# Optimization experiments

Hardware: AMD Instinct MI355X
Metric: run time of the kernel (lower is better)

Reference implementation:

```python
import jax, jax.numpy as jnp
import numpy as np
import math

EMBED_DIM = 256
N_HEAD = 8
N_LEVELS = 4
N_POINTS = 4
HEAD_DIM = EMBED_DIM // N_HEAD
TOTAL_POINTS = N_HEAD * N_LEVELS * N_POINTS
SPATIAL = np.array([[100, 100], [50, 50], [25, 25], [13, 13]], dtype=np.int32)
BS = 2
LEN_Q = int(SPATIAL.prod(1).sum())  # 13294, encoder self-attention
LEN_V = LEN_Q


def setup_inputs() -> dict:
    key = jax.random.key(0)
    ks = jax.random.split(key, 12)
    s = 1.0 / math.sqrt(EMBED_DIM)
    inp = {
        'query': jax.random.normal(ks[0], (BS, LEN_Q, EMBED_DIM), jnp.float32),
        'reference_points': jax.random.uniform(ks[1], (BS, LEN_Q, N_LEVELS, 2), jnp.float32),
        'value': jax.random.normal(ks[2], (BS, LEN_V, EMBED_DIM), jnp.float32),
        'value_spatial_shapes': jnp.asarray(SPATIAL),
        'W_value': jax.random.normal(ks[3], (EMBED_DIM, EMBED_DIM), jnp.float32) * s,
        'b_value': jnp.zeros((EMBED_DIM,), jnp.float32),
        'W_off': jax.random.normal(ks[4], (TOTAL_POINTS * 2, EMBED_DIM), jnp.float32) * 0.01,
        'b_off': jax.random.normal(ks[5], (TOTAL_POINTS * 2,), jnp.float32),
        'W_attn': jax.random.normal(ks[6], (TOTAL_POINTS, EMBED_DIM), jnp.float32) * s,
        'b_attn': jnp.zeros((TOTAL_POINTS,), jnp.float32),
        'W_out': jax.random.normal(ks[7], (EMBED_DIM, EMBED_DIM), jnp.float32) * s,
        'b_out': jnp.zeros((EMBED_DIM,), jnp.float32),
        'zeta': jnp.ones((1, 1, 1, HEAD_DIM), jnp.float32),  # search_type='embed'
    }
    return inp


def _grid_sample_bilinear(img, gx, gy):
    """img: [B,H,W,c]; gx,gy: [B,Q,P] normalized to [-1,1].
    align_corners=False, padding_mode='zeros' (matches F.grid_sample)."""
    B, H, W, c = img.shape
    x = (gx + 1.0) * (0.5 * W) - 0.5
    y = (gy + 1.0) * (0.5 * H) - 0.5
    x0 = jnp.floor(x)
    y0 = jnp.floor(y)
    wx = (x - x0)[..., None]
    wy = (y - y0)[..., None]
    flat = img.reshape(B, H * W, c)

    def gather(xi, yi):
        m = (xi >= 0) & (xi < W) & (yi >= 0) & (yi < H)
        xi_c = jnp.clip(xi, 0, W - 1).astype(jnp.int32)
        yi_c = jnp.clip(yi, 0, H - 1).astype(jnp.int32)
        idx = (yi_c * W + xi_c).reshape(B, -1, 1)
        v = jnp.take_along_axis(flat, idx, axis=1).reshape(B, *xi.shape[1:], c)
        return v * m[..., None]

    v00 = gather(x0, y0)
    v01 = gather(x0 + 1, y0)
    v10 = gather(x0, y0 + 1)
    v11 = gather(x0 + 1, y0 + 1)
    return (v00 * (1 - wx) * (1 - wy) + v01 * wx * (1 - wy)
            + v10 * (1 - wx) * wy + v11 * wx * wy)


def reference(query, reference_points, value, value_spatial_shapes,
              W_value, b_value, W_off, b_off, W_attn, b_attn, W_out, b_out, zeta):
    bs, Len_q, _ = query.shape
    Len_v = value.shape[1]
    shapes = np.asarray(value_spatial_shapes)  # static ints

    # value projection + sparse gate (zeta, not pruned/searched)
    v = value @ W_value.T + b_value
    v = v.reshape(bs, Len_v, N_HEAD, HEAD_DIM) * zeta  # [bs,Lv,h,c]

    # sampling offsets and attention weights from query
    off = (query @ W_off.T + b_off).reshape(bs, Len_q, N_HEAD, N_LEVELS, N_POINTS, 2)
    attn = (query @ W_attn.T + b_attn).reshape(bs, Len_q, N_HEAD, N_LEVELS * N_POINTS)
    attn = jax.nn.softmax(attn, axis=-1).reshape(bs, Len_q, N_HEAD, N_LEVELS, N_POINTS)

    # reference_points last dim == 2 branch
    normalizer = jnp.asarray(shapes[:, ::-1], jnp.float32).reshape(1, 1, 1, N_LEVELS, 1, 2)  # (W,H)
    loc = reference_points.reshape(bs, Len_q, 1, N_LEVELS, 1, 2) + off / normalizer
    grids = 2.0 * loc - 1.0  # [bs,Lq,h,L,P,2]

    B = bs * N_HEAD
    out = jnp.zeros((B, Len_q, HEAD_DIM), jnp.float32)
    start = 0
    for lvl in range(N_LEVELS):
        h, w = int(shapes[lvl, 0]), int(shapes[lvl, 1])
        # [bs, h*w, nh, c] -> [bs*nh, h, w, c]
        v_l = v[:, start:start + h * w].transpose(0, 2, 1, 3).reshape(B, h, w, HEAD_DIM)
        g = grids[:, :, :, lvl].transpose(0, 2, 1, 3, 4).reshape(B, Len_q, N_POINTS, 2)
        samp = _grid_sample_bilinear(v_l, g[..., 0], g[..., 1])  # [B,Lq,P,c]
        a_l = attn[:, :, :, lvl].transpose(0, 2, 1, 3).reshape(B, Len_q, N_POINTS)
        out = out + jnp.einsum('bqpc,bqp->bqc', samp, a_l)
        start += h * w

    out = out.reshape(bs, N_HEAD, Len_q, HEAD_DIM).transpose(0, 2, 1, 3).reshape(bs, Len_q, EMBED_DIM)
    return out @ W_out.T + b_out
```

## Files before the change

### kernel.cpp

```cpp
#include <hip/hip_runtime.h>


#define LQ    13294
#define NTOK  26588
#define CHUNK 3324
#define NE    6806528

typedef unsigned short ushort_t;
typedef __attribute__((ext_vector_type(8))) short short8;
typedef __attribute__((ext_vector_type(4))) float float4_t;
typedef __attribute__((ext_vector_type(2))) unsigned int uint2_t;

__device__ __forceinline__ ushort_t f2b(float f) {
    unsigned int x = __float_as_uint(f);
    return (ushort_t)((x + 0x7fffu + ((x >> 16) & 1u)) >> 16);
}

__device__ __forceinline__ void cvt_seg(const float* __restrict__ s,
                                        ushort_t* __restrict__ d,
                                        int n4, int gid, int stride) {
    const float4_t* s4 = (const float4_t*)s;
    for (int i = gid; i < n4; i += stride) {
        float4_t f = s4[i];
        ushort4 o;
        o.x = f2b(f.x); o.y = f2b(f.y); o.z = f2b(f.z); o.w = f2b(f.w);
        *(ushort4*)(d + (long)i * 4) = o;
    }
}

__global__ __launch_bounds__(256) void cvt_k(
    const float* q, const float* v, const float* Wv, const float* Wo,
    const float* Wa, const float* Wout,
    ushort_t* q_bf, ushort_t* v_bf, ushort_t* Wv_bf, ushort_t* WoWa_bf,
    ushort_t* Wout_bf)
{
    const int gid = blockIdx.x * 256 + threadIdx.x;
    const int stride = gridDim.x * 256;
    cvt_seg(q,    q_bf,            NE / 4,     gid, stride);
    cvt_seg(v,    v_bf,            NE / 4,     gid, stride);
    cvt_seg(Wv,   WoWa_bf ? Wv_bf : Wv_bf, 65536 / 4, gid, stride);
    cvt_seg(Wo,   WoWa_bf,         65536 / 4,  gid, stride);
    cvt_seg(Wa,   WoWa_bf + 65536, 32768 / 4,  gid, stride);
    cvt_seg(Wout, Wout_bf,         65536 / 4,  gid, stride);
}

__device__ __forceinline__ void gemm_tile(
    const ushort_t* __restrict__ A,
    const ushort_t* __restrict__ W,
    int m0, int n0, int M,
    ushort_t* As, ushort_t* Bs, float4_t acc[2][4])
{
    const int tid = threadIdx.x;
    const int w  = tid >> 6;
    const int ln = tid & 63;
    const int sr = tid >> 2;
    const int sc = (tid & 3) * 8;

    for (int k0 = 0; k0 < 256; k0 += 32) {
        #pragma unroll
        for (int rr = 0; rr < 128; rr += 64) {
            int m = m0 + sr + rr;
            short8 pk = {};
            if (m < M) pk = *(const short8*)(A + (long)m * 256 + k0 + sc);
            *(short8*)(As + (sr + rr) * 40 + sc) = pk;
        }
        *(short8*)(Bs + sr * 40 + sc) =
            *(const short8*)(W + (long)(n0 + sr) * 256 + k0 + sc);
        __syncthreads();

        const int krow = (ln >> 4) * 8;
        short8 af[2], bfr[4];
        #pragma unroll
        for (int i = 0; i < 2; i++)
            af[i] = *(const short8*)(As + (w * 32 + i * 16 + (ln & 15)) * 40 + krow);
        #pragma unroll
        for (int j = 0; j < 4; j++)
            bfr[j] = *(const short8*)(Bs + (j * 16 + (ln & 15)) * 40 + krow);
        #pragma unroll
        for (int i = 0; i < 2; i++)
            #pragma unroll
            for (int j = 0; j < 4; j++)
                acc[i][j] = __builtin_amdgcn_mfma_f32_16x16x32_bf16(af[i], bfr[j], acc[i][j], 0, 0, 0);
        __syncthreads();
    }
}

__global__ __launch_bounds__(256) void gemm_fused_k(
    const ushort_t* __restrict__ q_bf, const ushort_t* __restrict__ v_bf,
    const ushort_t* __restrict__ Wv,   const ushort_t* __restrict__ WoWa,
    const float* __restrict__ b_value, const float* __restrict__ b_off,
    const float* __restrict__ b_attn,  const float* __restrict__ zeta,
    ushort_t* __restrict__ vproj, float* __restrict__ oa)
{
    __shared__ __align__(16) ushort_t As[128 * 40];
    __shared__ __align__(16) ushort_t Bs[64 * 40];

    const int z = blockIdx.z;
    const int bid = blockIdx.x;
    int x, y;
    if (z == 0) {
        if (bid >= 832) return;
        int id = (bid & 7) * 104 + (bid >> 3);
        x = id >> 2; y = id & 3;
    } else {
        int id = (bid & 7) * 156 + (bid >> 3);
        x = id / 6; y = id - x * 6;
    }
    const int m0 = x * 128;
    const int n0 = y * 64;
    const ushort_t* A = z ? q_bf : v_bf;
    const ushort_t* W = z ? WoWa : Wv;

    float4_t acc[2][4] = {};
    gemm_tile(A, W, m0, n0, NTOK, As, Bs, acc);

    const int tid = threadIdx.x;
    const int w = tid >> 6, ln = tid & 63;
    const int col = ln & 15;
    const int rq  = (ln >> 4) * 4;
    #pragma unroll
    for (int j = 0; j < 4; j++) {
        int n = n0 + j * 16 + col;
        if (z == 0) {
            float bz = b_value[n];
            float zz = zeta[n & 31];
            #pragma unroll
            for (int i = 0; i < 2; i++) {
                #pragma unroll
                for (int r = 0; r < 4; r++) {
                    int m = m0 + w * 32 + i * 16 + rq + r;
                    if (m < NTOK) vproj[(long)m * 256 + n] = f2b((acc[i][j][r] + bz) * zz);
                }
            }
        } else {
            float bz = (n < 256) ? b_off[n] : b_attn[n - 256];
            #pragma unroll
            for (int i = 0; i < 2; i++) {
                #pragma unroll
                for (int r = 0; r < 4; r++) {
                    int m = m0 + w * 32 + i * 16 + rq + r;
                    if (m < NTOK) oa[(long)m * 384 + n] = acc[i][j][r] + bz;
                }
            }
        }
    }
}

__global__ __launch_bounds__(256) void gemm_out_k(
    const ushort_t* __restrict__ A,
    const ushort_t* __restrict__ W,
    const float* __restrict__ bias,
    float* __restrict__ C)
{
    __shared__ __align__(16) ushort_t As[128 * 40];
    __shared__ __align__(16) ushort_t Bs[64 * 40];

    const int bid = blockIdx.x;
    int id = (bid & 7) * 104 + (bid >> 3);
    const int m0 = (id >> 2) * 128;
    const int n0 = (id & 3) * 64;

    float4_t acc[2][4] = {};
    gemm_tile(A, W, m0, n0, NTOK, As, Bs, acc);

    const int tid = threadIdx.x;
    const int w = tid >> 6, ln = tid & 63;
    const int col = ln & 15;
    const int rq  = (ln >> 4) * 4;
    #pragma unroll
    for (int j = 0; j < 4; j++) {
        int n = n0 + j * 16 + col;
        float bz = bias[n];
        #pragma unroll
        for (int i = 0; i < 2; i++) {
            #pragma unroll
            for (int r = 0; r < 4; r++) {
                int m = m0 + w * 32 + i * 16 + rq + r;
                if (m < NTOK) C[(long)m * 256 + n] = acc[i][j][r] + bz;
            }
        }
    }
}

__global__ __launch_bounds__(512) void sample_k(
    const float* __restrict__ refp,
    const ushort_t* __restrict__ v,
    const float* __restrict__ oa,
    ushort_t* __restrict__ outp)
{
    __shared__ int   p_ofs[128][4];
    __shared__ float p_w[128][4];
    const int bid = blockIdx.x;
    const int t = (bid & 7) * CHUNK + (bid >> 3);
    if (t >= NTOK) return;
    const int b = (t >= LQ) ? 1 : 0;
    const int tid = threadIdx.x;

    if (tid < 128) {
        const int h = tid >> 4, pi = tid & 15;
        const int lvl = pi >> 2;
        const int Wi  = (lvl == 0) ? 100 : (lvl == 1) ? 50 : (lvl == 2) ? 25 : 13;
        const int st  = (lvl == 0) ? 0 : (lvl == 1) ? 10000 : (lvl == 2) ? 12500 : 13125;
        const float Wf = (float)Wi;

        float lg = oa[(long)t * 384 + 256 + h * 16 + pi];
        float smax = lg;
        #pragma unroll
        for (int d = 1; d < 16; d <<= 1) smax = fmaxf(smax, __shfl_xor(smax, d, 64));
        float ex = __expf(lg - smax);
        float sm = ex;
        #pragma unroll
        for (int d = 1; d < 16; d <<= 1) sm += __shfl_xor(sm, d, 64);
        const float a = ex / sm;

        float ox = oa[(long)t * 384 + h * 32 + pi * 2];
        float oy = oa[(long)t * 384 + h * 32 + pi * 2 + 1];
        float rx = refp[(long)t * 8 + lvl * 2];
        float ry = refp[(long)t * 8 + lvl * 2 + 1];

        float x = rx * Wf + ox - 0.5f;
        float y = ry * Wf + oy - 0.5f;
        float xf = floorf(x), yf = floorf(y);
        float wx = x - xf, wy = y - yf;
        int x0 = (int)xf, y0 = (int)yf;

        float mx0 = ((unsigned)x0       < (unsigned)Wi) ? (1.f - wx) : 0.f;
        float mx1 = ((unsigned)(x0 + 1) < (unsigned)Wi) ? wx         : 0.f;
        float my0 = ((unsigned)y0       < (unsigned)Wi) ? (1.f - wy) * a : 0.f;
        float my1 = ((unsigned)(y0 + 1) < (unsigned)Wi) ? wy * a         : 0.f;
        int x0c = min(max(x0, 0), Wi - 1);
        int x1c = min(max(x0 + 1, 0), Wi - 1);
        int y0c = min(max(y0, 0), Wi - 1);
        int y1c = min(max(y0 + 1, 0), Wi - 1);

        int r0 = st + y0c * Wi, r1 = st + y1c * Wi;
        p_ofs[tid][0] = (r0 + x0c) << 9;
        p_ofs[tid][1] = (r0 + x1c) << 9;
        p_ofs[tid][2] = (r1 + x0c) << 9;
        p_ofs[tid][3] = (r1 + x1c) << 9;
        p_w[tid][0] = mx0 * my0;
        p_w[tid][1] = mx1 * my0;
        p_w[tid][2] = mx0 * my1;
        p_w[tid][3] = mx1 * my1;
    }
    __syncthreads();

    const int h = tid >> 6, ln = tid & 63, g = ln & 7, s = ln >> 3;
    const char* vb = (const char*)(v + ((long)b * LQ) * 256 + h * 32 + g * 4);
    float4_t acc = {0.f, 0.f, 0.f, 0.f};

    #pragma unroll
    for (int it = 0; it < 2; it++) {
        const int task = h * 16 + it * 8 + s;
        int4     o  = *(const int4*)p_ofs[task];
        float4_t w4 = *(const float4_t*)p_w[task];
        uint2_t u00 = *(const uint2_t*)(vb + o.x);
        uint2_t u01 = *(const uint2_t*)(vb + o.y);
        uint2_t u10 = *(const uint2_t*)(vb + o.z);
        uint2_t u11 = *(const uint2_t*)(vb + o.w);
        acc[0] += w4.x * __uint_as_float(u00.x << 16)
                + w4.y * __uint_as_float(u01.x << 16)
                + w4.z * __uint_as_float(u10.x << 16)
                + w4.w * __uint_as_float(u11.x << 16);
        acc[1] += w4.x * __uint_as_float(u00.x & 0xffff0000u)
                + w4.y * __uint_as_float(u01.x & 0xffff0000u)
                + w4.z * __uint_as_float(u10.x & 0xffff0000u)
                + w4.w * __uint_as_float(u11.x & 0xffff0000u);
        acc[2] += w4.x * __uint_as_float(u00.y << 16)
                + w4.y * __uint_as_float(u01.y << 16)
                + w4.z * __uint_as_float(u10.y << 16)
                + w4.w * __uint_as_float(u11.y << 16);
        acc[3] += w4.x * __uint_as_float(u00.y & 0xffff0000u)
                + w4.y * __uint_as_float(u01.y & 0xffff0000u)
                + w4.z * __uint_as_float(u10.y & 0xffff0000u)
                + w4.w * __uint_as_float(u11.y & 0xffff0000u);
    }

    #pragma unroll
    for (int d = 32; d >= 8; d >>= 1) {
        acc.x += __shfl_down(acc.x, d, 64);
        acc.y += __shfl_down(acc.y, d, 64);
        acc.z += __shfl_down(acc.z, d, 64);
        acc.w += __shfl_down(acc.w, d, 64);
    }
    if (s == 0) {
        ushort4 o;
        o.x = f2b(acc.x); o.y = f2b(acc.y); o.z = f2b(acc.z); o.w = f2b(acc.w);
        *(ushort4*)(outp + (long)t * 256 + h * 32 + g * 4) = o;
    }
}

extern "C" void kernel_launch(void* const* d_in, const int* in_sizes, int n_in,
                              void* d_out, int out_size, void* d_ws, size_t ws_size,
                              hipStream_t stream)
{
    char* ws = (char*)d_ws;
    ushort_t* vproj   = (ushort_t*)ws;
    float*    oa      = (float*)(ws + (long)NE * 2);
    ushort_t* q_bf    = (ushort_t*)(ws + (long)NE * 2 + (long)NTOK * 1536);
    ushort_t* outpre  = q_bf;
    ushort_t* v_bf    = q_bf + NE;
    ushort_t* Wv_bf   = v_bf + NE;
    ushort_t* WoWa_bf = Wv_bf + 65536;
    ushort_t* Wout_bf = WoWa_bf + 98304;

    cvt_k<<<1024, 256, 0, stream>>>(
        (const float*)d_in[0], (const float*)d_in[2], (const float*)d_in[4],
        (const float*)d_in[6], (const float*)d_in[8], (const float*)d_in[10],
        q_bf, v_bf, Wv_bf, WoWa_bf, Wout_bf);

    gemm_fused_k<<<dim3(1248, 1, 2), 256, 0, stream>>>(
        q_bf, v_bf, Wv_bf, WoWa_bf,
        (const float*)d_in[5], (const float*)d_in[7], (const float*)d_in[9],
        (const float*)d_in[12], vproj, oa);

    sample_k<<<8 * CHUNK, 512, 0, stream>>>(
        (const float*)d_in[1], vproj, oa, outpre);

    gemm_out_k<<<832, 256, 0, stream>>>(
        outpre, Wout_bf, (const float*)d_in[11], (float*)d_out);
}
```

Before: 242.0 us.

## Load GEMM tiles directly to LDS and batch four tokens per sampling block

The GEMM tile loader now uses global_load_lds to move 16-byte chunks straight from global memory into unpadded LDS tiles. This removes the register round-trip and the M bounds check, so the last tile reads rows past NTOK from adjacent workspace memory, though its stores stay guarded. The unpadded row stride of 32 may also cause LDS bank conflicts on fragment reads. The sampling kernel now handles four tokens per 512-thread block, so every thread computes sampling offsets and weights and each lane accumulates eight points instead of two, with a shorter shuffle reduction.

```diff
diff --git a/kernel.cpp b/kernel.cpp
--- a/kernel.cpp
+++ b/kernel.cpp
@@ -3,7 +3,6 @@
 
 #define LQ    13294
 #define NTOK  26588
-#define CHUNK 3324
 #define NE    6806528
 
 typedef unsigned short ushort_t;
@@ -14,6 +13,12 @@
 __device__ __forceinline__ ushort_t f2b(float f) {
     unsigned int x = __float_as_uint(f);
     return (ushort_t)((x + 0x7fffu + ((x >> 16) & 1u)) >> 16);
+}
+
+__device__ __forceinline__ void gload16(const void* g, void* l) {
+    __builtin_amdgcn_global_load_lds(
+        (const __attribute__((address_space(1))) unsigned int*)g,
+        (__attribute__((address_space(3))) unsigned int*)l, 16, 0, 0);
 }
 
 __device__ __forceinline__ void cvt_seg(const float* __restrict__ s,
@@ -38,7 +43,7 @@
     const int stride = gridDim.x * 256;
     cvt_seg(q,    q_bf,            NE / 4,     gid, stride);
     cvt_seg(v,    v_bf,            NE / 4,     gid, stride);
-    cvt_seg(Wv,   WoWa_bf ? Wv_bf : Wv_bf, 65536 / 4, gid, stride);
+    cvt_seg(Wv,   Wv_bf,           65536 / 4,  gid, stride);
     cvt_seg(Wo,   WoWa_bf,         65536 / 4,  gid, stride);
     cvt_seg(Wa,   WoWa_bf + 65536, 32768 / 4,  gid, stride);
     cvt_seg(Wout, Wout_bf,         65536 / 4,  gid, stride);
@@ -47,35 +52,38 @@
 __device__ __forceinline__ void gemm_tile(
     const ushort_t* __restrict__ A,
     const ushort_t* __restrict__ W,
-    int m0, int n0, int M,
+    int m0, int n0,
     ushort_t* As, ushort_t* Bs, float4_t acc[2][4])
 {
     const int tid = threadIdx.x;
     const int w  = tid >> 6;
     const int ln = tid & 63;
-    const int sr = tid >> 2;
-    const int sc = (tid & 3) * 8;
+    const int lr = ln >> 2;
+    const int lc = (ln & 3) * 8;
+
+    ushort_t* lA0 = As + (w * 2 + 0) * 512;
+    ushort_t* lA1 = As + (w * 2 + 1) * 512;
+    ushort_t* lB  = Bs + w * 512;
+    const ushort_t* gA0 = A + (long)(m0 + w * 32 + lr) * 256 + lc;
+    const ushort_t* gA1 = gA0 + 16 * 256;
+    const ushort_t* gB  = W + (long)(n0 + w * 16 + lr) * 256 + lc;
+
+    const int krow = (ln >> 4) * 8;
+    const int fr   = ln & 15;
 
     for (int k0 = 0; k0 < 256; k0 += 32) {
-        #pragma unroll
-        for (int rr = 0; rr < 128; rr += 64) {
-            int m = m0 + sr + rr;
-            short8 pk = {};
-            if (m < M) pk = *(const short8*)(A + (long)m * 256 + k0 + sc);
-            *(short8*)(As + (sr + rr) * 40 + sc) = pk;
-        }
-        *(short8*)(Bs + sr * 40 + sc) =
-            *(const short8*)(W + (long)(n0 + sr) * 256 + k0 + sc);
+        gload16(gA0 + k0, lA0);
+        gload16(gA1 + k0, lA1);
+        gload16(gB  + k0, lB);
         __syncthreads();
 
-        const int krow = (ln >> 4) * 8;
         short8 af[2], bfr[4];
         #pragma unroll
         for (int i = 0; i < 2; i++)
-            af[i] = *(const short8*)(As + (w * 32 + i * 16 + (ln & 15)) * 40 + krow);
+            af[i] = *(const short8*)(As + (w * 32 + i * 16 + fr) * 32 + krow);
         #pragma unroll
         for (int j = 0; j < 4; j++)
-            bfr[j] = *(const short8*)(Bs + (j * 16 + (ln & 15)) * 40 + krow);
+            bfr[j] = *(const short8*)(Bs + (j * 16 + fr) * 32 + krow);
         #pragma unroll
         for (int i = 0; i < 2; i++)
             #pragma unroll
@@ -92,8 +100,8 @@
     const float* __restrict__ b_attn,  const float* __restrict__ zeta,
     ushort_t* __restrict__ vproj, float* __restrict__ oa)
 {
-    __shared__ __align__(16) ushort_t As[128 * 40];
-    __shared__ __align__(16) ushort_t Bs[64 * 40];
+    __shared__ __align__(16) ushort_t As[128 * 32];
+    __shared__ __align__(16) ushort_t Bs[64 * 32];
 
     const int z = blockIdx.z;
     const int bid = blockIdx.x;
@@ -108,11 +116,9 @@
     }
     const int m0 = x * 128;
     const int n0 = y * 64;
-    const ushort_t* A = z ? q_bf : v_bf;
-    const ushort_t* W = z ? WoWa : Wv;
 
     float4_t acc[2][4] = {};
-    gemm_tile(A, W, m0, n0, NTOK, As, Bs, acc);
+    gemm_tile(z ? q_bf : v_bf, z ? WoWa : Wv, m0, n0, As, Bs, acc);
 
     const int tid = threadIdx.x;
     const int w = tid >> 6, ln = tid & 63;
@@ -152,8 +158,8 @@
     const float* __restrict__ bias,
     float* __restrict__ C)
 {
-    __shared__ __align__(16) ushort_t As[128 * 40];
-    __shared__ __align__(16) ushort_t Bs[64 * 40];
+    __shared__ __align__(16) ushort_t As[128 * 32];
+    __shared__ __align__(16) ushort_t Bs[64 * 32];
 
     const int bid = blockIdx.x;
     int id = (bid & 7) * 104 + (bid >> 3);
@@ -161,7 +167,7 @@
     const int n0 = (id & 3) * 64;
 
     float4_t acc[2][4] = {};
-    gemm_tile(A, W, m0, n0, NTOK, As, Bs, acc);
+    gemm_tile(A, W, m0, n0, As, Bs, acc);
 
     const int tid = threadIdx.x;
     const int w = tid >> 6, ln = tid & 63;
@@ -188,22 +194,21 @@
     const float* __restrict__ oa,
     ushort_t* __restrict__ outp)
 {
-    __shared__ int   p_ofs[128][4];
-    __shared__ float p_w[128][4];
-    const int bid = blockIdx.x;
-    const int t = (bid & 7) * CHUNK + (bid >> 3);
-    if (t >= NTOK) return;
-    const int b = (t >= LQ) ? 1 : 0;
+    __shared__ int   p_ofs[512][4];
+    __shared__ float p_w[512][4];
     const int tid = threadIdx.x;
-
-    if (tid < 128) {
-        const int h = tid >> 4, pi = tid & 15;
+    const int t0 = blockIdx.x * 4;
+
+    {
+        const int tok = tid >> 7, wt = tid & 127;
+        const long t = t0 + tok;
+        const int h = wt >> 4, pi = wt & 15;
         const int lvl = pi >> 2;
         const int Wi  = (lvl == 0) ? 100 : (lvl == 1) ? 50 : (lvl == 2) ? 25 : 13;
         const int st  = (lvl == 0) ? 0 : (lvl == 1) ? 10000 : (lvl == 2) ? 12500 : 13125;
         const float Wf = (float)Wi;
 
-        float lg = oa[(long)t * 384 + 256 + h * 16 + pi];
+        float lg = oa[t * 384 + 256 + h * 16 + pi];
         float smax = lg;
         #pragma unroll
         for (int d = 1; d < 16; d <<= 1) smax = fmaxf(smax, __shfl_xor(smax, d, 64));
@@ -213,10 +218,10 @@
         for (int d = 1; d < 16; d <<= 1) sm += __shfl_xor(sm, d, 64);
         const float a = ex / sm;
 
-        float ox = oa[(long)t * 384 + h * 32 + pi * 2];
-        float oy = oa[(long)t * 384 + h * 32 + pi * 2 + 1];
-        float rx = refp[(long)t * 8 + lvl * 2];
-        float ry = refp[(long)t * 8 + lvl * 2 + 1];
+        float ox = oa[t * 384 + h * 32 + pi * 2];
+        float oy = oa[t * 384 + h * 32 + pi * 2 + 1];
+        float rx = refp[t * 8 + lvl * 2];
+        float ry = refp[t * 8 + lvl * 2 + 1];
 
         float x = rx * Wf + ox - 0.5f;
         float y = ry * Wf + oy - 0.5f;
@@ -245,15 +250,18 @@
     }
     __syncthreads();
 
-    const int h = tid >> 6, ln = tid & 63, g = ln & 7, s = ln >> 3;
+    const int tok = tid >> 7, wt = tid & 127;
+    const long t = t0 + tok;
+    const int b = (t >= LQ) ? 1 : 0;
+    const int h = wt >> 4, s = (wt >> 3) & 1, g = wt & 7;
     const char* vb = (const char*)(v + ((long)b * LQ) * 256 + h * 32 + g * 4);
+    const int base = tok * 128 + h * 16 + s * 8;
     float4_t acc = {0.f, 0.f, 0.f, 0.f};
 
-    #pragma unroll
-    for (int it = 0; it < 2; it++) {
-        const int task = h * 16 + it * 8 + s;
-        int4     o  = *(const int4*)p_ofs[task];
-        float4_t w4 = *(const float4_t*)p_w[task];
+    #pragma unroll 4
+    for (int p = 0; p < 8; p++) {
+        int4     o  = *(const int4*)p_ofs[base + p];
+        float4_t w4 = *(const float4_t*)p_w[base + p];
         uint2_t u00 = *(const uint2_t*)(vb + o.x);
         uint2_t u01 = *(const uint2_t*)(vb + o.y);
         uint2_t u10 = *(const uint2_t*)(vb + o.z);
@@ -276,17 +284,15 @@
                 + w4.w * __uint_as_float(u11.y & 0xffff0000u);
     }
 
-    #pragma unroll
-    for (int d = 32; d >= 8; d >>= 1) {
-        acc.x += __shfl_down(acc.x, d, 64);
-        acc.y += __shfl_down(acc.y, d, 64);
-        acc.z += __shfl_down(acc.z, d, 64);
-        acc.w += __shfl_down(acc.w, d, 64);
-    }
+    acc.x += __shfl_down(acc.x, 8, 64);
+    acc.y += __shfl_down(acc.y, 8, 64);
+    acc.z += __shfl_down(acc.z, 8, 64);
+    acc.w += __shfl_down(acc.w, 8, 64);
+
     if (s == 0) {
         ushort4 o;
         o.x = f2b(acc.x); o.y = f2b(acc.y); o.z = f2b(acc.z); o.w = f2b(acc.w);
-        *(ushort4*)(outp + (long)t * 256 + h * 32 + g * 4) = o;
+        *(ushort4*)(outp + t * 256 + h * 32 + g * 4) = o;
     }
 }
 
@@ -314,7 +320,7 @@
         (const float*)d_in[5], (const float*)d_in[7], (const float*)d_in[9],
         (const float*)d_in[12], vproj, oa);
 
-    sample_k<<<8 * CHUNK, 512, 0, stream>>>(
+    sample_k<<<6647, 512, 0, stream>>>(
         (const float*)d_in[1], vproj, oa, outpre);
 
     gemm_out_k<<<832, 256, 0, stream>>>(
```

New measurement: 224.5 us. -7.2%, faster.
